# Kernel tuning notes

Measured on AMD Instinct MI355X. Metric: run time of the kernel, lower is better.

The kernel has to match this reference:

```python
import math
import jax, jax.numpy as jnp
import numpy as np

B, L, D, H = 2, 2048, 512, 8
HD = D // H
PADDING_IDX = 0


def _sinusoid_table(num_embeddings, dim, padding_idx):
    # matches RelativeSinusoidalPositionalEmbedding.get_embedding
    half = dim // 2
    inv = math.log(10000.0) / (half - 1)
    freqs = jnp.exp(jnp.arange(half, dtype=jnp.float32) * (-inv))
    ang = jnp.arange(num_embeddings, dtype=jnp.float32)[:, None] * freqs[None, :]
    emb = jnp.concatenate([jnp.sin(ang), jnp.cos(ang)], axis=1)  # [N, dim]
    return emb.at[padding_idx].set(0.0)


def _rel_pos_embed(seq_len):
    # RelativeEmbedding.forward: init table size 513 (origin_shift=257); since
    # padding_idx + seq_len > 257 it regenerates with num_embeddings = 2*seq_len,
    # origin_shift = seq_len. All static at trace time.
    init_origin = 512 // 2 + 1
    if PADDING_IDX + seq_len > init_origin:
        num = (PADDING_IDX + seq_len) * 2
        origin = num // 2
    else:
        num = 512 + 1
        origin = init_origin
    table = _sinusoid_table(num, HD, PADDING_IDX)
    positions = jnp.arange(-seq_len, seq_len) + origin  # [2L]
    return table[positions]  # [2L, HD]


def _shift(BD):
    # [B,H,L,2L] -> [B,H,L,L], Transformer-XL relative shift
    b, h, l, _ = BD.shape
    BD = jnp.concatenate([BD, jnp.zeros((b, h, l, 1), BD.dtype)], axis=-1)
    BD = BD.reshape(b, h, -1, l)[:, :, :-1].reshape(b, h, l, -1)
    return BD[:, :, :, l:]


def setup_inputs() -> dict:
    key = jax.random.key(0)
    ks = jax.random.split(key, 7)
    s = 1.0 / math.sqrt(D)
    return {
        "q": jax.random.normal(ks[0], (B, L, D), jnp.float32),
        "k": jax.random.normal(ks[1], (B, L, D), jnp.float32),
        "mask": jnp.ones((B, L, L), jnp.int32),
        "Wq": jax.random.normal(ks[2], (D, D), jnp.float32) * s,
        "Wkv": jax.random.normal(ks[3], (2 * D, D), jnp.float32) * s,
        "Wr": jax.random.normal(ks[4], (HD, HD), jnp.float32) * (1.0 / math.sqrt(HD)),
        "r_r_bias": jax.random.normal(ks[5], (H, HD), jnp.float32) * 0.1,
        "r_w_bias": jax.random.normal(ks[6], (H, HD), jnp.float32) * 0.1,
    }


def reference(q, k, mask, Wq, Wkv, Wr, r_r_bias, r_w_bias):
    b, l, d = q.shape
    scale = math.sqrt(HD)

    pos = _rel_pos_embed(l)                # [2L, HD]
    r = pos @ Wr.T                          # [2L, HD]

    qp = q @ Wq.T                           # [B,L,D]
    kv = k @ Wkv.T                          # [B,L,2D]
    kk, vv = jnp.split(kv, 2, axis=-1)

    qh = qp.reshape(b, l, H, HD).transpose(0, 2, 1, 3)  # [B,H,L,HD]
    kh = kk.reshape(b, l, H, HD).transpose(0, 2, 1, 3)
    vh = vv.reshape(b, l, H, HD).transpose(0, 2, 1, 3)

    rw_head_q = qh + r_r_bias[None, :, None, :]
    AC = jnp.einsum('bnqd,bnkd->bnqk', rw_head_q, kh)        # [B,H,L,L]
    D_ = jnp.einsum('nd,ld->nl', r_w_bias, r)[None, :, None, :]  # [1,H,1,2L]
    B_ = jnp.einsum('bnqd,ld->bnql', qh, r)                  # [B,H,L,2L]
    BD = _shift(B_ + D_)                                      # [B,H,L,L]

    attn = (AC + BD) / scale
    attn = jnp.where(mask[:, None, :, :] == 0, -jnp.inf, attn)
    attn = jax.nn.softmax(attn, axis=-1)

    out = jnp.einsum('bnqk,bnkd->bnqd', attn, vh)
    out = out.transpose(0, 2, 1, 3).reshape(b, l, d)
    return (out, attn)
```

## Files before the change

### kernel.cpp

```cpp
#include <hip/hip_runtime.h>
#include <math.h>

#define NL 2048
#define N2L 4096

typedef __attribute__((ext_vector_type(8))) short bf16x8;
typedef __attribute__((ext_vector_type(4))) float f32x4;
#define MFMA(a,b,c) __builtin_amdgcn_mfma_f32_16x16x32_bf16((a),(b),(c),0,0,0)

__device__ __forceinline__ unsigned short bf16_rne(float x){
  unsigned int u = __float_as_uint(x);
  u += 0x7FFFu + ((u>>16)&1u);
  return (unsigned short)(u>>16);
}
__device__ __forceinline__ float bf16_to_f(unsigned short h){
  return __uint_as_float(((unsigned int)h)<<16);
}

__global__ __launch_bounds__(256) void split_kernel(
    const float* __restrict__ q, const float* __restrict__ k,
    const float* __restrict__ Wq, const float* __restrict__ Wkv,
    unsigned short* __restrict__ qsh, unsigned short* __restrict__ qsl,
    unsigned short* __restrict__ ksh, unsigned short* __restrict__ ksl,
    unsigned short* __restrict__ wqh, unsigned short* __restrict__ wql,
    unsigned short* __restrict__ wkh, unsigned short* __restrict__ wkl) {
  const int C1 = 524288, C2 = 1048576, C3 = 1114112, C4 = 1245184;
  for (int i = blockIdx.x * blockDim.x + threadIdx.x; i < C4; i += gridDim.x * blockDim.x) {
    const float* src; unsigned short *dh, *dl; int j;
    if (i < C1)      { src = q;   dh = qsh; dl = qsl; j = i; }
    else if (i < C2) { src = k;   dh = ksh; dl = ksl; j = i - C1; }
    else if (i < C3) { src = Wq;  dh = wqh; dl = wql; j = i - C2; }
    else             { src = Wkv; dh = wkh; dl = wkl; j = i - C3; }
    float4 v = reinterpret_cast<const float4*>(src)[j];
    unsigned short h0 = bf16_rne(v.x), h1 = bf16_rne(v.y), h2 = bf16_rne(v.z), h3 = bf16_rne(v.w);
    unsigned short l0 = bf16_rne(v.x - bf16_to_f(h0));
    unsigned short l1 = bf16_rne(v.y - bf16_to_f(h1));
    unsigned short l2 = bf16_rne(v.z - bf16_to_f(h2));
    unsigned short l3 = bf16_rne(v.w - bf16_to_f(h3));
    reinterpret_cast<uint2*>(dh)[j] = make_uint2((unsigned)h0 | ((unsigned)h1 << 16),
                                                 (unsigned)h2 | ((unsigned)h3 << 16));
    reinterpret_cast<uint2*>(dl)[j] = make_uint2((unsigned)l0 | ((unsigned)l1 << 16),
                                                 (unsigned)l2 | ((unsigned)l3 << 16));
  }
}

__global__ void build_r_kernel(const float* __restrict__ Wr,
                               unsigned short* __restrict__ rh,
                               unsigned short* __restrict__ rl) {
  int n = blockIdx.x;
  int t = threadIdx.x;
  __shared__ float pos[64];
  float v = 0.f;
  if (n != 0) {
    int j = t & 31;
    float inv = logf(10000.f) * (1.0f / 31.0f);
    float freq = expf(-inv * (float)j);
    float ang = (float)n * freq;
    v = (t < 32) ? sinf(ang) : cosf(ang);
  }
  pos[t] = v;
  __syncthreads();
  float acc = 0.f;
  const float* wrow = Wr + t * 64;
  #pragma unroll
  for (int j = 0; j < 64; ++j) acc += pos[j] * wrow[j];
  unsigned short hh = bf16_rne(acc);
  rh[n * 64 + t] = hh;
  rl[n * 64 + t] = bf16_rne(acc - bf16_to_f(hh));
}

__global__ __launch_bounds__(256) void proj_kernel(
    const unsigned short* __restrict__ qsh, const unsigned short* __restrict__ qsl,
    const unsigned short* __restrict__ ksh, const unsigned short* __restrict__ ksl,
    const unsigned short* __restrict__ wqh, const unsigned short* __restrict__ wql,
    const unsigned short* __restrict__ wkh, const unsigned short* __restrict__ wkl,
    const float* __restrict__ rrb, const float* __restrict__ rwb,
    unsigned short* __restrict__ qAh, unsigned short* __restrict__ qAl,
    unsigned short* __restrict__ qBh, unsigned short* __restrict__ qBl,
    unsigned short* __restrict__ khh, unsigned short* __restrict__ khl,
    unsigned short* __restrict__ vTh, unsigned short* __restrict__ vTl) {
  int tid = threadIdx.x;
  int w = tid >> 6, lane = tid & 63, li = lane & 15, g = lane >> 4;
  int bx = blockIdx.x, by = blockIdx.y;
  f32x4 acc[4];
  #pragma unroll
  for (int i = 0; i < 4; ++i) { acc[i][0]=0.f; acc[i][1]=0.f; acc[i][2]=0.f; acc[i][3]=0.f; }

  if (by < 16) {
    int n0 = by * 64, m0 = bx * 64;
    const unsigned short* Xh = (n0 < 512) ? qsh : ksh;
    const unsigned short* Xl = (n0 < 512) ? qsl : ksl;
    const unsigned short* Wh = (n0 < 512) ? (wqh + (size_t)n0 * 512) : (wkh + (size_t)(n0 - 512) * 512);
    const unsigned short* Wl = (n0 < 512) ? (wql + (size_t)n0 * 512) : (wkl + (size_t)(n0 - 512) * 512);
    int rowm = m0 + 16 * w + li;
    for (int ks = 0; ks < 16; ++ks) {
      int d0 = ks * 32 + 8 * g;
      bf16x8 ah = *(const bf16x8*)(Xh + (size_t)rowm * 512 + d0);
      bf16x8 al = *(const bf16x8*)(Xl + (size_t)rowm * 512 + d0);
      #pragma unroll
      for (int nt = 0; nt < 4; ++nt) {
        bf16x8 bh_ = *(const bf16x8*)(Wh + (size_t)(16 * nt + li) * 512 + d0);
        bf16x8 bl_ = *(const bf16x8*)(Wl + (size_t)(16 * nt + li) * 512 + d0);
        acc[nt] = MFMA(ah, bh_, acc[nt]);
        acc[nt] = MFMA(al, bh_, acc[nt]);
        acc[nt] = MFMA(ah, bl_, acc[nt]);
      }
    }
    if (n0 < 512) {
      int h = n0 >> 6;
      #pragma unroll
      for (int nt = 0; nt < 4; ++nt) {
        int d = 16 * nt + li;
        float rrv = rrb[h * 64 + d], rwv = rwb[h * 64 + d];
        #pragma unroll
        for (int r = 0; r < 4; ++r) {
          int m = m0 + 16 * w + 4 * g + r;
          int b = m >> 11, lt = m & 2047;
          size_t base = (((size_t)(b * 8 + h)) * 2048 + lt) * 64 + d;
          float a1 = acc[nt][r] + rrv;
          unsigned short h1 = bf16_rne(a1);
          qAh[base] = h1; qAl[base] = bf16_rne(a1 - bf16_to_f(h1));
          float a2 = acc[nt][r] + rwv;
          unsigned short h2 = bf16_rne(a2);
          qBh[base] = h2; qBl[base] = bf16_rne(a2 - bf16_to_f(h2));
        }
      }
    } else {
      int h = (n0 - 512) >> 6;
      #pragma unroll
      for (int nt = 0; nt < 4; ++nt) {
        int d = 16 * nt + li;
        #pragma unroll
        for (int r = 0; r < 4; ++r) {
          int m = m0 + 16 * w + 4 * g + r;
          int b = m >> 11, lt = m & 2047;
          size_t base = (((size_t)(b * 8 + h)) * 2048 + lt) * 64 + d;
          unsigned short h1 = bf16_rne(acc[nt][r]);
          khh[base] = h1; khl[base] = bf16_rne(acc[nt][r] - bf16_to_f(h1));
        }
      }
    }
  } else {
    int fy = by - 16, m0 = bx * 64, f0 = fy * 64;
    const unsigned short* Ah = wkh + (size_t)(512 + f0 + 16 * w + li) * 512;
    const unsigned short* Al = wkl + (size_t)(512 + f0 + 16 * w + li) * 512;
    for (int ks = 0; ks < 16; ++ks) {
      int d0 = ks * 32 + 8 * g;
      bf16x8 ah = *(const bf16x8*)(Ah + d0);
      bf16x8 al = *(const bf16x8*)(Al + d0);
      #pragma unroll
      for (int nt = 0; nt < 4; ++nt) {
        bf16x8 bh_ = *(const bf16x8*)(ksh + (size_t)(m0 + 16 * nt + li) * 512 + d0);
        bf16x8 bl_ = *(const bf16x8*)(ksl + (size_t)(m0 + 16 * nt + li) * 512 + d0);
        acc[nt] = MFMA(ah, bh_, acc[nt]);
        acc[nt] = MFMA(al, bh_, acc[nt]);
        acc[nt] = MFMA(ah, bl_, acc[nt]);
      }
    }
    int h = fy;
    #pragma unroll
    for (int nt = 0; nt < 4; ++nt) {
      int m = m0 + 16 * nt + li;
      int b = m >> 11, lt = m & 2047;
      #pragma unroll
      for (int r = 0; r < 4; ++r) {
        int d = 16 * w + 4 * g + r;
        size_t base = (((size_t)(b * 8 + h)) * 64 + d) * 2048 + lt;
        unsigned short h1 = bf16_rne(acc[nt][r]);
        vTh[base] = h1; vTl[base] = bf16_rne(acc[nt][r] - bf16_to_f(h1));
      }
    }
  }
}

__global__ __launch_bounds__(256) void attn_kernel(
    const unsigned short* __restrict__ qAh, const unsigned short* __restrict__ qAl,
    const unsigned short* __restrict__ qBh, const unsigned short* __restrict__ qBl,
    const unsigned short* __restrict__ khh, const unsigned short* __restrict__ khl,
    const unsigned short* __restrict__ vTh, const unsigned short* __restrict__ vTl,
    const unsigned short* __restrict__ rh, const unsigned short* __restrict__ rl,
    const int* __restrict__ mask, float* __restrict__ outp, float* __restrict__ attnp) {
  __shared__ float Tlds[96 * 34];
  __shared__ unsigned int Plds[2048];
  __shared__ float mw[4][32], lw[4][32], mf[32], rlf[32];

  int tid = threadIdx.x;
  int w = tid >> 6, lane = tid & 63, li = lane & 15, g = lane >> 4;
  int q0 = blockIdx.x * 32;
  int bh = blockIdx.y, b = bh >> 3, h = bh & 7;
  const unsigned short* qAhp = qAh + (size_t)bh * 131072;
  const unsigned short* qAlp = qAl + (size_t)bh * 131072;
  const unsigned short* qBhp = qBh + (size_t)bh * 131072;
  const unsigned short* qBlp = qBl + (size_t)bh * 131072;
  const unsigned short* khhp = khh + (size_t)bh * 131072;
  const unsigned short* khlp = khl + (size_t)bh * 131072;
  const unsigned short* vThp = vTh + (size_t)bh * 131072;
  const unsigned short* vTlp = vTl + (size_t)bh * 131072;
  float* attn_bh = attnp + (size_t)bh * NL * NL;
  const int* mask_b = mask + (size_t)b * NL * NL;

  bf16x8 fAh[2][2], fAl[2][2], fBh[2][2], fBl[2][2];
  #pragma unroll
  for (int nt = 0; nt < 2; ++nt)
    #pragma unroll
    for (int ks = 0; ks < 2; ++ks) {
      size_t o = (size_t)(q0 + 16 * nt + li) * 64 + 32 * ks + 8 * g;
      fAh[nt][ks] = *(const bf16x8*)(qAhp + o);
      fAl[nt][ks] = *(const bf16x8*)(qAlp + o);
      fBh[nt][ks] = *(const bf16x8*)(qBhp + o);
      fBl[nt][ks] = *(const bf16x8*)(qBlp + o);
    }
  float mrun[2] = {-3.0e38f, -3.0e38f}, lrun[2] = {0.f, 0.f};

  for (int kt = 0; kt < 32; ++kt) {
    int k0 = kt * 64;
    int krow = k0 + 16 * w + li;
    f32x4 accS[2];
    #pragma unroll
    for (int i = 0; i < 2; ++i) { accS[i][0]=0.f; accS[i][1]=0.f; accS[i][2]=0.f; accS[i][3]=0.f; }
    #pragma unroll
    for (int ks = 0; ks < 2; ++ks) {
      size_t o = (size_t)krow * 64 + 32 * ks + 8 * g;
      bf16x8 ah = *(const bf16x8*)(khhp + o);
      bf16x8 al = *(const bf16x8*)(khlp + o);
      #pragma unroll
      for (int nt = 0; nt < 2; ++nt) {
        accS[nt] = MFMA(ah, fAh[nt][ks], accS[nt]);
        accS[nt] = MFMA(al, fAh[nt][ks], accS[nt]);
        accS[nt] = MFMA(ah, fAl[nt][ks], accS[nt]);
      }
    }
    int nlo = k0 - q0 + 2017;
    f32x4 accT[3];
    #pragma unroll
    for (int i = 0; i < 3; ++i) { accT[i][0]=0.f; accT[i][1]=0.f; accT[i][2]=0.f; accT[i][3]=0.f; }
    #pragma unroll
    for (int p = 0; p < 3; ++p) {
      int pi = w * 3 + p, jt = pi >> 1, ntp = pi & 1;
      int rrow = nlo + jt * 16 + li;
      if (rrow > 4095) rrow = 4095;
      #pragma unroll
      for (int ks = 0; ks < 2; ++ks) {
        size_t o = (size_t)rrow * 64 + 32 * ks + 8 * g;
        bf16x8 ah = *(const bf16x8*)(rh + o);
        bf16x8 al = *(const bf16x8*)(rl + o);
        accT[p] = MFMA(ah, fBh[ntp][ks], accT[p]);
        accT[p] = MFMA(al, fBh[ntp][ks], accT[p]);
        accT[p] = MFMA(ah, fBl[ntp][ks], accT[p]);
      }
    }
    __syncthreads();
    #pragma unroll
    for (int p = 0; p < 3; ++p) {
      int pi = w * 3 + p, jt = pi >> 1, ntp = pi & 1;
      #pragma unroll
      for (int r = 0; r < 4; ++r)
        Tlds[(jt * 16 + 4 * g + r) * 34 + ntp * 16 + li] = accT[p][r];
    }
    __syncthreads();
    #pragma unroll
    for (int nt = 0; nt < 2; ++nt) {
      int ql_ = 16 * nt + li;
      int qg = q0 + ql_;
      int kb = k0 + 16 * w + 4 * g;
      int4 mv = *(const int4*)(mask_b + (size_t)qg * NL + kb);
      float sv[4];
      #pragma unroll
      for (int r = 0; r < 4; ++r) {
        int kl = 16 * w + 4 * g + r;
        sv[r] = (accS[nt][r] + Tlds[(kl - ql_ + 31) * 34 + ql_]) * 0.125f;
      }
      if (mv.x == 0) sv[0] = -1e30f;
      if (mv.y == 0) sv[1] = -1e30f;
      if (mv.z == 0) sv[2] = -1e30f;
      if (mv.w == 0) sv[3] = -1e30f;
      *(float4*)(attn_bh + (size_t)qg * NL + kb) = make_float4(sv[0], sv[1], sv[2], sv[3]);
      float vmax = fmaxf(fmaxf(sv[0], sv[1]), fmaxf(sv[2], sv[3]));
      vmax = fmaxf(vmax, __shfl_xor(vmax, 16));
      vmax = fmaxf(vmax, __shfl_xor(vmax, 32));
      float sum = __expf(sv[0] - vmax) + __expf(sv[1] - vmax) +
                  __expf(sv[2] - vmax) + __expf(sv[3] - vmax);
      sum += __shfl_xor(sum, 16);
      sum += __shfl_xor(sum, 32);
      float mo = mrun[nt];
      float mn = fmaxf(mo, vmax);
      lrun[nt] = lrun[nt] * __expf(mo - mn) + sum * __expf(vmax - mn);
      mrun[nt] = mn;
    }
  }
  if (lane < 16) {
    mw[w][li] = mrun[0]; lw[w][li] = lrun[0];
    mw[w][16 + li] = mrun[1]; lw[w][16 + li] = lrun[1];
  }
  __syncthreads();
  if (tid < 32) {
    float m = mw[0][tid];
    m = fmaxf(m, mw[1][tid]); m = fmaxf(m, mw[2][tid]); m = fmaxf(m, mw[3][tid]);
    float l = lw[0][tid] * __expf(mw[0][tid] - m) + lw[1][tid] * __expf(mw[1][tid] - m) +
              lw[2][tid] * __expf(mw[2][tid] - m) + lw[3][tid] * __expf(mw[3][tid] - m);
    mf[tid] = m; rlf[tid] = 1.0f / l;
  }
  __syncthreads();

  f32x4 accO[2];
  #pragma unroll
  for (int i = 0; i < 2; ++i) { accO[i][0]=0.f; accO[i][1]=0.f; accO[i][2]=0.f; accO[i][3]=0.f; }
  int qlc = tid >> 3;
  int kc = (tid & 7) * 8;
  float mm = mf[qlc], rr = rlf[qlc];
  unsigned int woff = (unsigned)(qlc * 128 + ((kc * 2) ^ ((qlc & 7) << 4)));

  for (int kt = 0; kt < 32; ++kt) {
    int k0 = kt * 64;
    float* pp = attn_bh + (size_t)(q0 + qlc) * NL + k0 + kc;
    float4 sa = *(float4*)pp;
    float4 sb = *(float4*)(pp + 4);
    float p0 = __expf(sa.x - mm) * rr, p1 = __expf(sa.y - mm) * rr;
    float p2 = __expf(sa.z - mm) * rr, p3 = __expf(sa.w - mm) * rr;
    float p4 = __expf(sb.x - mm) * rr, p5 = __expf(sb.y - mm) * rr;
    float p6 = __expf(sb.z - mm) * rr, p7 = __expf(sb.w - mm) * rr;
    *(float4*)pp = make_float4(p0, p1, p2, p3);
    *(float4*)(pp + 4) = make_float4(p4, p5, p6, p7);
    unsigned short h0 = bf16_rne(p0), h1 = bf16_rne(p1), h2 = bf16_rne(p2), h3 = bf16_rne(p3);
    unsigned short h4 = bf16_rne(p4), h5 = bf16_rne(p5), h6 = bf16_rne(p6), h7 = bf16_rne(p7);
    unsigned short e0 = bf16_rne(p0 - bf16_to_f(h0)), e1 = bf16_rne(p1 - bf16_to_f(h1));
    unsigned short e2 = bf16_rne(p2 - bf16_to_f(h2)), e3 = bf16_rne(p3 - bf16_to_f(h3));
    unsigned short e4 = bf16_rne(p4 - bf16_to_f(h4)), e5 = bf16_rne(p5 - bf16_to_f(h5));
    unsigned short e6 = bf16_rne(p6 - bf16_to_f(h6)), e7 = bf16_rne(p7 - bf16_to_f(h7));
    __syncthreads();
    *(uint4*)((char*)Plds + woff) =
        make_uint4((unsigned)h0 | ((unsigned)h1 << 16), (unsigned)h2 | ((unsigned)h3 << 16),
                   (unsigned)h4 | ((unsigned)h5 << 16), (unsigned)h6 | ((unsigned)h7 << 16));
    *(uint4*)((char*)Plds + 4096 + woff) =
        make_uint4((unsigned)e0 | ((unsigned)e1 << 16), (unsigned)e2 | ((unsigned)e3 << 16),
                   (unsigned)e4 | ((unsigned)e5 << 16), (unsigned)e6 | ((unsigned)e7 << 16));
    __syncthreads();
    #pragma unroll
    for (int ks = 0; ks < 2; ++ks) {
      size_t vo = (size_t)(16 * w + li) * NL + k0 + 32 * ks + 8 * g;
      bf16x8 vh_ = *(const bf16x8*)(vThp + vo);
      bf16x8 vl_ = *(const bf16x8*)(vTlp + vo);
      #pragma unroll
      for (int nt = 0; nt < 2; ++nt) {
        unsigned int ro = (unsigned)((16 * nt + li) * 128 + (((32 * ks + 8 * g) * 2) ^ ((li & 7) << 4)));
        bf16x8 ph = *(const bf16x8*)((const char*)Plds + ro);
        bf16x8 pl = *(const bf16x8*)((const char*)Plds + 4096 + ro);
        accO[nt] = MFMA(vh_, ph, accO[nt]);
        accO[nt] = MFMA(vl_, ph, accO[nt]);
        accO[nt] = MFMA(vh_, pl, accO[nt]);
      }
    }
  }
  #pragma unroll
  for (int nt = 0; nt < 2; ++nt) {
    int qg = q0 + 16 * nt + li;
    int d = 16 * w + 4 * g;
    *(float4*)(outp + ((size_t)b * NL + qg) * 512 + h * 64 + d) =
        make_float4(accO[nt][0], accO[nt][1], accO[nt][2], accO[nt][3]);
  }
}

extern "C" void kernel_launch(void* const* d_in, const int* in_sizes, int n_in,
                              void* d_out, int out_size, void* d_ws, size_t ws_size,
                              hipStream_t stream) {
  const float* q    = (const float*)d_in[0];
  const float* k    = (const float*)d_in[1];
  const int*   mask = (const int*)d_in[2];
  const float* Wq   = (const float*)d_in[3];
  const float* Wkv  = (const float*)d_in[4];
  const float* Wr   = (const float*)d_in[5];
  const float* rrb  = (const float*)d_in[6];
  const float* rwb  = (const float*)d_in[7];

  float* outp  = (float*)d_out;
  float* attnp = outp + (size_t)2 * NL * 512;

  unsigned short* W = (unsigned short*)d_ws;
  const size_t RHI = 0,            RLO = RHI + 262144;
  const size_t QSH = RLO + 262144, QSL = QSH + 2097152;
  const size_t KSH = QSL + 2097152, KSL = KSH + 2097152;
  const size_t WQH = KSL + 2097152, WQL = WQH + 262144;
  const size_t WKH = WQL + 262144,  WKL = WKH + 524288;
  const size_t QAH = WKL + 524288,  QAL = QAH + 2097152;
  const size_t QBH = QAL + 2097152, QBL = QBH + 2097152;
  const size_t KHH = QBL + 2097152, KHL = KHH + 2097152;
  const size_t VTH = KHL + 2097152, VTL = VTH + 2097152;

  hipLaunchKernelGGL(split_kernel, dim3(1024), dim3(256), 0, stream,
                     q, k, Wq, Wkv, W+QSH, W+QSL, W+KSH, W+KSL, W+WQH, W+WQL, W+WKH, W+WKL);
  hipLaunchKernelGGL(build_r_kernel, dim3(N2L), dim3(64), 0, stream, Wr, W+RHI, W+RLO);
  hipLaunchKernelGGL(proj_kernel, dim3(64, 24), dim3(256), 0, stream,
                     W+QSH, W+QSL, W+KSH, W+KSL, W+WQH, W+WQL, W+WKH, W+WKL, rrb, rwb,
                     W+QAH, W+QAL, W+QBH, W+QBL, W+KHH, W+KHL, W+VTH, W+VTL);
  hipLaunchKernelGGL(attn_kernel, dim3(64, 16), dim3(256), 0, stream,
                     W+QAH, W+QAL, W+QBH, W+QBL, W+KHH, W+KHL, W+VTH, W+VTL,
                     W+RHI, W+RLO, mask, outp, attnp);
}
```

Baseline: 667.3 us.

## Recompute attention scores in second pass instead of round-tripping through global memory

Pass one no longer writes raw scores to the attn buffer. Instead it stages each score tile in LDS and computes per-row max and sum there, with the per-row reduction now spread across 8 lanes. Pass two recomputes the QK and relative-position MFMAs, applies the mask, and writes only the final probabilities. This removes one global write and one global read of the large B×H×L×L score matrix, at the cost of doing the score MFMA work twice and adding LDS usage and extra syncs.

```diff
diff --git a/kernel.cpp b/kernel.cpp
--- a/kernel.cpp
+++ b/kernel.cpp
@@ -181,11 +181,12 @@
     const unsigned short* __restrict__ rh, const unsigned short* __restrict__ rl,
     const int* __restrict__ mask, float* __restrict__ outp, float* __restrict__ attnp) {
   __shared__ float Tlds[96 * 34];
+  __shared__ float Slds[2048];
   __shared__ unsigned int Plds[2048];
-  __shared__ float mw[4][32], lw[4][32], mf[32], rlf[32];
 
   int tid = threadIdx.x;
   int w = tid >> 6, lane = tid & 63, li = lane & 15, g = lane >> 4;
+  int qlc = tid >> 3, jc = tid & 7, kc = jc * 8;
   int q0 = blockIdx.x * 32;
   int bh = blockIdx.y, b = bh >> 3, h = bh & 7;
   const unsigned short* qAhp = qAh + (size_t)bh * 131072;
@@ -196,8 +197,8 @@
   const unsigned short* khlp = khl + (size_t)bh * 131072;
   const unsigned short* vThp = vTh + (size_t)bh * 131072;
   const unsigned short* vTlp = vTl + (size_t)bh * 131072;
-  float* attn_bh = attnp + (size_t)bh * NL * NL;
-  const int* mask_b = mask + (size_t)b * NL * NL;
+  const int* mrow = mask + (size_t)b * NL * NL + (size_t)(q0 + qlc) * NL;
+  float* arow = attnp + (size_t)bh * NL * NL + (size_t)(q0 + qlc) * NL;
 
   bf16x8 fAh[2][2], fAl[2][2], fBh[2][2], fBl[2][2];
   #pragma unroll
@@ -210,9 +211,11 @@
       fBh[nt][ks] = *(const bf16x8*)(qBhp + o);
       fBl[nt][ks] = *(const bf16x8*)(qBlp + o);
     }
-  float mrun[2] = {-3.0e38f, -3.0e38f}, lrun[2] = {0.f, 0.f};
-
-  for (int kt = 0; kt < 32; ++kt) {
+
+  unsigned int sread0 = (unsigned)(qlc * 256 + (((2 * jc) * 16) ^ ((qlc & 7) << 4)));
+  unsigned int sread1 = (unsigned)(qlc * 256 + (((2 * jc + 1) * 16) ^ ((qlc & 7) << 4)));
+
+  auto compute_s = [&](int kt) {
     int k0 = kt * 64;
     int krow = k0 + 16 * w + li;
     f32x4 accS[2];
@@ -235,8 +238,8 @@
     #pragma unroll
     for (int i = 0; i < 3; ++i) { accT[i][0]=0.f; accT[i][1]=0.f; accT[i][2]=0.f; accT[i][3]=0.f; }
     #pragma unroll
-    for (int p = 0; p < 3; ++p) {
-      int pi = w * 3 + p, jt = pi >> 1, ntp = pi & 1;
+    for (int pp = 0; pp < 3; ++pp) {
+      int pi = w * 3 + pp, jt = pi >> 1, ntp = pi & 1;
       int rrow = nlo + jt * 16 + li;
       if (rrow > 4095) rrow = 4095;
       #pragma unroll
@@ -244,90 +247,91 @@
         size_t o = (size_t)rrow * 64 + 32 * ks + 8 * g;
         bf16x8 ah = *(const bf16x8*)(rh + o);
         bf16x8 al = *(const bf16x8*)(rl + o);
-        accT[p] = MFMA(ah, fBh[ntp][ks], accT[p]);
-        accT[p] = MFMA(al, fBh[ntp][ks], accT[p]);
-        accT[p] = MFMA(ah, fBl[ntp][ks], accT[p]);
+        accT[pp] = MFMA(ah, fBh[ntp][ks], accT[pp]);
+        accT[pp] = MFMA(al, fBh[ntp][ks], accT[pp]);
+        accT[pp] = MFMA(ah, fBl[ntp][ks], accT[pp]);
       }
     }
     __syncthreads();
     #pragma unroll
-    for (int p = 0; p < 3; ++p) {
-      int pi = w * 3 + p, jt = pi >> 1, ntp = pi & 1;
+    for (int pp = 0; pp < 3; ++pp) {
+      int pi = w * 3 + pp, jt = pi >> 1, ntp = pi & 1;
       #pragma unroll
       for (int r = 0; r < 4; ++r)
-        Tlds[(jt * 16 + 4 * g + r) * 34 + ntp * 16 + li] = accT[p][r];
+        Tlds[(jt * 16 + 4 * g + r) * 34 + ntp * 16 + li] = accT[pp][r];
     }
     __syncthreads();
     #pragma unroll
     for (int nt = 0; nt < 2; ++nt) {
       int ql_ = 16 * nt + li;
-      int qg = q0 + ql_;
-      int kb = k0 + 16 * w + 4 * g;
-      int4 mv = *(const int4*)(mask_b + (size_t)qg * NL + kb);
       float sv[4];
       #pragma unroll
       for (int r = 0; r < 4; ++r) {
         int kl = 16 * w + 4 * g + r;
         sv[r] = (accS[nt][r] + Tlds[(kl - ql_ + 31) * 34 + ql_]) * 0.125f;
       }
-      if (mv.x == 0) sv[0] = -1e30f;
-      if (mv.y == 0) sv[1] = -1e30f;
-      if (mv.z == 0) sv[2] = -1e30f;
-      if (mv.w == 0) sv[3] = -1e30f;
-      *(float4*)(attn_bh + (size_t)qg * NL + kb) = make_float4(sv[0], sv[1], sv[2], sv[3]);
-      float vmax = fmaxf(fmaxf(sv[0], sv[1]), fmaxf(sv[2], sv[3]));
-      vmax = fmaxf(vmax, __shfl_xor(vmax, 16));
-      vmax = fmaxf(vmax, __shfl_xor(vmax, 32));
-      float sum = __expf(sv[0] - vmax) + __expf(sv[1] - vmax) +
-                  __expf(sv[2] - vmax) + __expf(sv[3] - vmax);
-      sum += __shfl_xor(sum, 16);
-      sum += __shfl_xor(sum, 32);
-      float mo = mrun[nt];
-      float mn = fmaxf(mo, vmax);
-      lrun[nt] = lrun[nt] * __expf(mo - mn) + sum * __expf(vmax - mn);
-      mrun[nt] = mn;
-    }
-  }
-  if (lane < 16) {
-    mw[w][li] = mrun[0]; lw[w][li] = lrun[0];
-    mw[w][16 + li] = mrun[1]; lw[w][16 + li] = lrun[1];
-  }
-  __syncthreads();
-  if (tid < 32) {
-    float m = mw[0][tid];
-    m = fmaxf(m, mw[1][tid]); m = fmaxf(m, mw[2][tid]); m = fmaxf(m, mw[3][tid]);
-    float l = lw[0][tid] * __expf(mw[0][tid] - m) + lw[1][tid] * __expf(mw[1][tid] - m) +
-              lw[2][tid] * __expf(mw[2][tid] - m) + lw[3][tid] * __expf(mw[3][tid] - m);
-    mf[tid] = m; rlf[tid] = 1.0f / l;
-  }
-  __syncthreads();
+      unsigned int so = (unsigned)(ql_ * 256 + (((4 * w + g) * 16) ^ ((ql_ & 7) << 4)));
+      *(float4*)((char*)Slds + so) = make_float4(sv[0], sv[1], sv[2], sv[3]);
+    }
+    __syncthreads();
+  };
+
+  float mrun = -3.0e38f, lrun = 0.f;
+  for (int kt = 0; kt < 32; ++kt) {
+    compute_s(kt);
+    int k0 = kt * 64;
+    int4 m1 = *(const int4*)(mrow + k0 + kc);
+    int4 m2 = *(const int4*)(mrow + k0 + kc + 4);
+    float4 sa = *(const float4*)((const char*)Slds + sread0);
+    float4 sb = *(const float4*)((const char*)Slds + sread1);
+    float v0 = m1.x ? sa.x : -1e30f, v1 = m1.y ? sa.y : -1e30f;
+    float v2 = m1.z ? sa.z : -1e30f, v3 = m1.w ? sa.w : -1e30f;
+    float v4 = m2.x ? sb.x : -1e30f, v5 = m2.y ? sb.y : -1e30f;
+    float v6 = m2.z ? sb.z : -1e30f, v7 = m2.w ? sb.w : -1e30f;
+    float tmax = fmaxf(fmaxf(fmaxf(v0, v1), fmaxf(v2, v3)),
+                       fmaxf(fmaxf(v4, v5), fmaxf(v6, v7)));
+    tmax = fmaxf(tmax, __shfl_xor(tmax, 1));
+    tmax = fmaxf(tmax, __shfl_xor(tmax, 2));
+    tmax = fmaxf(tmax, __shfl_xor(tmax, 4));
+    float ts = __expf(v0 - tmax) + __expf(v1 - tmax) + __expf(v2 - tmax) + __expf(v3 - tmax) +
+               __expf(v4 - tmax) + __expf(v5 - tmax) + __expf(v6 - tmax) + __expf(v7 - tmax);
+    ts += __shfl_xor(ts, 1);
+    ts += __shfl_xor(ts, 2);
+    ts += __shfl_xor(ts, 4);
+    float mn = fmaxf(mrun, tmax);
+    lrun = lrun * __expf(mrun - mn) + ts * __expf(tmax - mn);
+    mrun = mn;
+  }
+  float mm = mrun, rlv = 1.0f / lrun;
 
   f32x4 accO[2];
   #pragma unroll
   for (int i = 0; i < 2; ++i) { accO[i][0]=0.f; accO[i][1]=0.f; accO[i][2]=0.f; accO[i][3]=0.f; }
-  int qlc = tid >> 3;
-  int kc = (tid & 7) * 8;
-  float mm = mf[qlc], rr = rlf[qlc];
   unsigned int woff = (unsigned)(qlc * 128 + ((kc * 2) ^ ((qlc & 7) << 4)));
 
   for (int kt = 0; kt < 32; ++kt) {
+    compute_s(kt);
     int k0 = kt * 64;
-    float* pp = attn_bh + (size_t)(q0 + qlc) * NL + k0 + kc;
-    float4 sa = *(float4*)pp;
-    float4 sb = *(float4*)(pp + 4);
-    float p0 = __expf(sa.x - mm) * rr, p1 = __expf(sa.y - mm) * rr;
-    float p2 = __expf(sa.z - mm) * rr, p3 = __expf(sa.w - mm) * rr;
-    float p4 = __expf(sb.x - mm) * rr, p5 = __expf(sb.y - mm) * rr;
-    float p6 = __expf(sb.z - mm) * rr, p7 = __expf(sb.w - mm) * rr;
-    *(float4*)pp = make_float4(p0, p1, p2, p3);
-    *(float4*)(pp + 4) = make_float4(p4, p5, p6, p7);
+    int4 m1 = *(const int4*)(mrow + k0 + kc);
+    int4 m2 = *(const int4*)(mrow + k0 + kc + 4);
+    float4 sa = *(const float4*)((const char*)Slds + sread0);
+    float4 sb = *(const float4*)((const char*)Slds + sread1);
+    float p0 = m1.x ? __expf(sa.x - mm) * rlv : 0.f;
+    float p1 = m1.y ? __expf(sa.y - mm) * rlv : 0.f;
+    float p2 = m1.z ? __expf(sa.z - mm) * rlv : 0.f;
+    float p3 = m1.w ? __expf(sa.w - mm) * rlv : 0.f;
+    float p4 = m2.x ? __expf(sb.x - mm) * rlv : 0.f;
+    float p5 = m2.y ? __expf(sb.y - mm) * rlv : 0.f;
+    float p6 = m2.z ? __expf(sb.z - mm) * rlv : 0.f;
+    float p7 = m2.w ? __expf(sb.w - mm) * rlv : 0.f;
+    *(float4*)(arow + k0 + kc) = make_float4(p0, p1, p2, p3);
+    *(float4*)(arow + k0 + kc + 4) = make_float4(p4, p5, p6, p7);
     unsigned short h0 = bf16_rne(p0), h1 = bf16_rne(p1), h2 = bf16_rne(p2), h3 = bf16_rne(p3);
     unsigned short h4 = bf16_rne(p4), h5 = bf16_rne(p5), h6 = bf16_rne(p6), h7 = bf16_rne(p7);
     unsigned short e0 = bf16_rne(p0 - bf16_to_f(h0)), e1 = bf16_rne(p1 - bf16_to_f(h1));
     unsigned short e2 = bf16_rne(p2 - bf16_to_f(h2)), e3 = bf16_rne(p3 - bf16_to_f(h3));
     unsigned short e4 = bf16_rne(p4 - bf16_to_f(h4)), e5 = bf16_rne(p5 - bf16_to_f(h5));
     unsigned short e6 = bf16_rne(p6 - bf16_to_f(h6)), e7 = bf16_rne(p7 - bf16_to_f(h7));
-    __syncthreads();
     *(uint4*)((char*)Plds + woff) =
         make_uint4((unsigned)h0 | ((unsigned)h1 << 16), (unsigned)h2 | ((unsigned)h3 << 16),
                    (unsigned)h4 | ((unsigned)h5 << 16), (unsigned)h6 | ((unsigned)h7 << 16));
```

Result: slower. 782.2 us (+17.2%).
